# Kernel optimization log

Measured on AMD Instinct MI355X. Metric: run time of the kernel, lower is better.

Reference implementation:

```python
import jax, jax.numpy as jnp
import numpy as np

B, T, V, E, H = 4096, 128, 30, 256, 128

def setup_inputs() -> dict:
    key = jax.random.key(0)
    ks = jax.random.split(key, 12)
    inpt = jax.random.randint(ks[0], (B, T), 0, V, dtype=jnp.int32)
    h0 = jax.random.normal(ks[1], (B, H), dtype=jnp.float32)
    c0 = jax.random.normal(ks[2], (B, H), dtype=jnp.float32)
    mask_Y = jnp.ones((B, T), dtype=jnp.float32)
    s_e = 1.0
    s_l = 1.0 / np.sqrt(H)
    s_i = 1.0 / np.sqrt(E)
    emb = jax.random.normal(ks[3], (V, E), dtype=jnp.float32) * s_e
    W_ih = jax.random.normal(ks[4], (4 * H, E), dtype=jnp.float32) * s_i
    b_ih = jax.random.normal(ks[5], (4 * H,), dtype=jnp.float32) * s_i
    W_hh = jax.random.normal(ks[6], (4 * H, H), dtype=jnp.float32) * s_l
    b_hh = jax.random.normal(ks[7], (4 * H,), dtype=jnp.float32) * s_l
    W_lin = jax.random.normal(ks[8], (V, H), dtype=jnp.float32) * s_l
    b_lin = jax.random.normal(ks[9], (V,), dtype=jnp.float32) * s_l
    return {"inpt": inpt, "h0": h0, "c0": c0, "mask_Y": mask_Y, "beta": 1,
            "emb": emb, "W_ih": W_ih, "b_ih": b_ih, "W_hh": W_hh,
            "b_hh": b_hh, "W_lin": W_lin, "b_lin": b_lin}


def reference(inpt, h0, c0, mask_Y, beta, emb, W_ih, b_ih, W_hh, b_hh, W_lin, b_lin):
    # beta == 1 -> teacher forcing every step (u <= beta always), as in source.
    t_max = inpt.shape[1]
    # input tokens fed at steps t=0..t_max-2 are inpt[:, 0:t_max-1]
    x_emb = emb[inpt[:, :t_max - 1]]          # [B, T-1, E]
    xs = (jnp.swapaxes(x_emb, 0, 1),           # [T-1, B, E]
          inpt[:, 1:].T,                       # [T-1, B] true labels
          mask_Y[:, :t_max - 1].T)             # [T-1, B]

    def step(carry, xs_t):
        h, c = carry
        x, y, m = xs_t
        gates = x @ W_ih.T + b_ih + h @ W_hh.T + b_hh   # [B, 4H]
        i, f, g, o = jnp.split(gates, 4, axis=1)
        c2 = jax.nn.sigmoid(f) * c + jax.nn.sigmoid(i) * jnp.tanh(g)
        h2 = jax.nn.sigmoid(o) * jnp.tanh(c2)
        # -log(softmax(logits))[y] == -log_softmax(logits)[y]
        logp = jax.nn.log_softmax(h2 @ W_lin.T + b_lin, axis=1)  # [B, V]
        ce = -jnp.take_along_axis(logp, y[:, None], axis=1)[:, 0]
        return (h2, c2), jnp.sum(ce * m)

    _, step_losses = jax.lax.scan(step, (h0, c0), xs)
    return jnp.sum(step_losses) / jnp.sum(mask_Y)
```

## Files before the change

kernel.cpp:

```cpp
#include <hip/hip_runtime.h>


typedef __bf16 bf16x8 __attribute__((ext_vector_type(8)));
typedef float  f32x4  __attribute__((ext_vector_type(4)));

namespace {
constexpr int Bn = 4096, Tn = 128, Vn = 30, En = 256, Hn = 128, Gn = 512;
constexpr int WS_LOSS  = 0;
constexpr int WS_MASK  = 1;
constexpr int WS_XPROJ = 16;
constexpr int WS_WF_F  = WS_XPROJ + Vn * Gn;
}

__device__ __forceinline__ float fexp2(float x) { return __builtin_amdgcn_exp2f(x); }
__device__ __forceinline__ float frcp(float x)  { return __builtin_amdgcn_rcpf(x); }
__device__ __forceinline__ float sigf(float x)  { return frcp(1.f + fexp2(x * -1.44269504f)); }
__device__ __forceinline__ float tanh_(float x) { return 1.f - 2.f * frcp(fexp2(x * 2.88539008f) + 1.f); }

__global__ void k_wfrag(const float* __restrict__ W_hh, float* __restrict__ ws) {
  int fid = blockIdx.x * 256 + threadIdx.x;
  int l = fid & 63, kt = (fid >> 6) & 3, g = (fid >> 8) & 3, w = fid >> 10;
  int n  = (g * 8 + w) * 16 + (l & 15);
  int k0 = kt * 32 + (l >> 4) * 8;
  const float* src = W_hh + n * Hn + k0;
  union { __bf16 h[8]; uint4 u; } pk;
#pragma unroll
  for (int j = 0; j < 8; ++j) pk.h[j] = (__bf16)src[j];
  __bf16* wf = (__bf16*)(ws + WS_WF_F);
  *(uint4*)(wf + fid * 8) = pk.u;
}

__global__ void k_wlfrag(const float* __restrict__ W_lin, float* __restrict__ ws) {
  int fid = blockIdx.x * 256 + threadIdx.x;
  if (fid < 2) ws[fid] = 0.f;
  int l = fid & 63, kt = (fid >> 6) & 3, n = fid >> 8;
  int col = n * 16 + (l & 15);
  int k0  = kt * 32 + (l >> 4) * 8;
  union { __bf16 h[8]; uint4 u; } pk;
#pragma unroll
  for (int j = 0; j < 8; ++j)
    pk.h[j] = (col < Vn) ? (__bf16)W_lin[col * Hn + k0 + j] : (__bf16)0.f;
  __bf16* wf = (__bf16*)(ws + WS_WF_F);
  *(uint4*)(wf + 65536 + fid * 8) = pk.u;
}

__global__ void k_xproj(const float* __restrict__ emb, const float* __restrict__ W_ih,
                        const float* __restrict__ b_ih, const float* __restrict__ b_hh,
                        float* __restrict__ ws) {
  __shared__ __align__(16) float es[En];
  int v = blockIdx.x >> 1;
  int j = ((blockIdx.x & 1) << 8) + threadIdx.x;
  es[threadIdx.x] = emb[v * En + threadIdx.x];
  __syncthreads();
  float a = b_ih[j] + b_hh[j];
  const float* wr = W_ih + j * En;
#pragma unroll 4
  for (int e = 0; e < En; e += 4) {
    float4 w = *(const float4*)(wr + e);
    float4 x = *(const float4*)(es + e);
    a += x.x * w.x + x.y * w.y + x.z * w.z + x.w * w.w;
  }
  ws[WS_XPROJ + v * Gn + j] = a;
}

__global__ void k_mask(const float* __restrict__ m, float* __restrict__ ws) {
  float s = 0.f;
  for (int i = blockIdx.x * 256 + threadIdx.x; i < Bn * Tn; i += 128 * 256) s += m[i];
#pragma unroll
  for (int off = 32; off > 0; off >>= 1) s += __shfl_down(s, off, 64);
  __shared__ float r[4];
  int lane = threadIdx.x & 63, w = threadIdx.x >> 6;
  if (lane == 0) r[w] = s;
  __syncthreads();
  if (threadIdx.x == 0) atomicAdd(ws + WS_MASK, r[0] + r[1] + r[2] + r[3]);
}

__global__ __launch_bounds__(512, 1) void k_main(
    const int* __restrict__ inpt, const float* __restrict__ h0,
    const float* __restrict__ c0, const float* __restrict__ maskY,
    const float* __restrict__ b_lin, float* __restrict__ ws) {
  __shared__ __align__(16) __bf16 hbuf[2][16][136];
  __shared__ float logits[16][33];
  __shared__ int   tok[16][Tn];
  __shared__ float red[16];

  const float*  Xp  = ws + WS_XPROJ;
  const __bf16* wf  = (const __bf16*)(ws + WS_WF_F);
  const __bf16* wlf = wf + 65536;

  const int tid = threadIdx.x;
  const int w = tid >> 6, l = tid & 63, quad = l >> 4, lc = l & 15;
  const int row0 = blockIdx.x * 16;
  const int kh = w * 16 + lc;

  bf16x8 wfr[4][4];
#pragma unroll
  for (int g = 0; g < 4; ++g)
#pragma unroll
    for (int kt = 0; kt < 4; ++kt)
      wfr[g][kt] = __builtin_bit_cast(
          bf16x8, *(const uint4*)(wf + (((w * 4 + g) * 4 + kt) * 64 + l) * 8));

  bf16x8 wlr[4];
  if (w < 2) {
#pragma unroll
    for (int kt = 0; kt < 4; ++kt)
      wlr[kt] = __builtin_bit_cast(
          bf16x8, *(const uint4*)(wlf + ((w * 4 + kt) * 64 + l) * 8));
  }
  const float blv = (w < 2 && kh < Vn) ? b_lin[kh] : 0.f;

  for (int idx = tid; idx < 16 * Tn; idx += 512) {
    int r = idx >> 7, t = idx & 127;
    tok[r][t] = inpt[(row0 + r) * Tn + t];
  }
  for (int idx = tid; idx < 16 * Hn; idx += 512) {
    int r = idx >> 7, k = idx & 127;
    hbuf[0][r][k] = (__bf16)h0[(row0 + r) * Hn + k];
  }
  float creg[4];
#pragma unroll
  for (int p = 0; p < 4; ++p)
    creg[p] = c0[(row0 + quad * 4 + p) * Hn + kh];
  float ce_acc = 0.f;
  __syncthreads();

  int par = 0;
  for (int t = 0; t < Tn - 1; ++t) {
    const __bf16* hc = &hbuf[par][0][0];
    __bf16*       hn = &hbuf[par ^ 1][0][0];

    bf16x8 af[4];
#pragma unroll
    for (int kt = 0; kt < 4; ++kt)
      af[kt] = __builtin_bit_cast(
          bf16x8, *(const uint4*)(hc + lc * 136 + kt * 32 + quad * 8));

    float xv[4][4];
#pragma unroll
    for (int p = 0; p < 4; ++p) {
      const float* xr = Xp + tok[quad * 4 + p][t] * Gn + kh;
#pragma unroll
      for (int g = 0; g < 4; ++g) xv[p][g] = xr[g * 128];
    }

    f32x4 acc[4] = {{0, 0, 0, 0}, {0, 0, 0, 0}, {0, 0, 0, 0}, {0, 0, 0, 0}};
#pragma unroll
    for (int g = 0; g < 4; ++g)
#pragma unroll
      for (int kt = 0; kt < 4; ++kt)
        acc[g] = __builtin_amdgcn_mfma_f32_16x16x32_bf16(af[kt], wfr[g][kt], acc[g], 0, 0, 0);

#pragma unroll
    for (int p = 0; p < 4; ++p) {
      float gi = acc[0][p] + xv[p][0];
      float gf = acc[1][p] + xv[p][1];
      float gg = acc[2][p] + xv[p][2];
      float go = acc[3][p] + xv[p][3];
      float c2 = sigf(gf) * creg[p] + sigf(gi) * tanh_(gg);
      float h2 = sigf(go) * tanh_(c2);
      creg[p] = c2;
      hn[(quad * 4 + p) * 136 + kh] = (__bf16)h2;
    }
    __syncthreads();

    if (w < 2) {
      f32x4 lacc = {blv, blv, blv, blv};
#pragma unroll
      for (int kt = 0; kt < 4; ++kt) {
        bf16x8 a2 = __builtin_bit_cast(
            bf16x8, *(const uint4*)(hn + lc * 136 + kt * 32 + quad * 8));
        lacc = __builtin_amdgcn_mfma_f32_16x16x32_bf16(a2, wlr[kt], lacc, 0, 0, 0);
      }
      if (kh < Vn) {
#pragma unroll
        for (int p = 0; p < 4; ++p) logits[quad * 4 + p][kh] = lacc[p];
      }
    }
    __syncthreads();

    if (tid < 16) {
      float mx = -3.4e38f;
#pragma unroll
      for (int v = 0; v < Vn; ++v) mx = fmaxf(mx, logits[tid][v]);
      float s = 0.f;
#pragma unroll
      for (int v = 0; v < Vn; ++v) s += fexp2((logits[tid][v] - mx) * 1.44269504f);
      int y = tok[tid][t + 1];
      float ce = (mx + __logf(s)) - logits[tid][y];
      ce_acc += ce * maskY[(row0 + tid) * Tn + t];
    }
    par ^= 1;
  }

  if (tid < 16) red[tid] = ce_acc;
  __syncthreads();
  if (tid == 0) {
    float s = 0.f;
#pragma unroll
    for (int i = 0; i < 16; ++i) s += red[i];
    atomicAdd(ws + WS_LOSS, s);
  }
}

__global__ void k_final(const float* __restrict__ ws, float* __restrict__ out) {
  if (threadIdx.x == 0 && blockIdx.x == 0) out[0] = ws[WS_LOSS] / ws[WS_MASK];
}

extern "C" void kernel_launch(void* const* d_in, const int* in_sizes, int n_in,
                              void* d_out, int out_size, void* d_ws, size_t ws_size,
                              hipStream_t stream) {
  const int*   inpt  = (const int*)  d_in[0];
  const float* h0    = (const float*)d_in[1];
  const float* c0    = (const float*)d_in[2];
  const float* maskY = (const float*)d_in[3];
  const float* emb   = (const float*)d_in[5];
  const float* W_ih  = (const float*)d_in[6];
  const float* b_ih  = (const float*)d_in[7];
  const float* W_hh  = (const float*)d_in[8];
  const float* b_hh  = (const float*)d_in[9];
  const float* W_lin = (const float*)d_in[10];
  const float* b_lin = (const float*)d_in[11];
  float* ws  = (float*)d_ws;
  float* out = (float*)d_out;

  hipLaunchKernelGGL(k_wlfrag, dim3(2),   dim3(256), 0, stream, W_lin, ws);
  hipLaunchKernelGGL(k_wfrag,  dim3(32),  dim3(256), 0, stream, W_hh, ws);
  hipLaunchKernelGGL(k_xproj,  dim3(60),  dim3(256), 0, stream, emb, W_ih, b_ih, b_hh, ws);
  hipLaunchKernelGGL(k_mask,   dim3(128), dim3(256), 0, stream, maskY, ws);
  hipLaunchKernelGGL(k_main,   dim3(256), dim3(512), 0, stream, inpt, h0, c0, maskY, b_lin, ws);
  hipLaunchKernelGGL(k_final,  dim3(1),   dim3(64),  0, stream, ws, out);
}
```

Measured before the change: 272.0 us.

## Add dedicated softmax warp, fuse setup kernels, prefetch gate inputs, drop a barrier

```diff
diff --git a/kernel.cpp b/kernel.cpp
--- a/kernel.cpp
+++ b/kernel.cpp
@@ -17,74 +17,61 @@
 __device__ __forceinline__ float sigf(float x)  { return frcp(1.f + fexp2(x * -1.44269504f)); }
 __device__ __forceinline__ float tanh_(float x) { return 1.f - 2.f * frcp(fexp2(x * 2.88539008f) + 1.f); }
 
-__global__ void k_wfrag(const float* __restrict__ W_hh, float* __restrict__ ws) {
-  int fid = blockIdx.x * 256 + threadIdx.x;
-  int l = fid & 63, kt = (fid >> 6) & 3, g = (fid >> 8) & 3, w = fid >> 10;
-  int n  = (g * 8 + w) * 16 + (l & 15);
-  int k0 = kt * 32 + (l >> 4) * 8;
-  const float* src = W_hh + n * Hn + k0;
-  union { __bf16 h[8]; uint4 u; } pk;
-#pragma unroll
-  for (int j = 0; j < 8; ++j) pk.h[j] = (__bf16)src[j];
-  __bf16* wf = (__bf16*)(ws + WS_WF_F);
-  *(uint4*)(wf + fid * 8) = pk.u;
-}
-
-__global__ void k_wlfrag(const float* __restrict__ W_lin, float* __restrict__ ws) {
-  int fid = blockIdx.x * 256 + threadIdx.x;
-  if (fid < 2) ws[fid] = 0.f;
-  int l = fid & 63, kt = (fid >> 6) & 3, n = fid >> 8;
-  int col = n * 16 + (l & 15);
-  int k0  = kt * 32 + (l >> 4) * 8;
-  union { __bf16 h[8]; uint4 u; } pk;
-#pragma unroll
-  for (int j = 0; j < 8; ++j)
-    pk.h[j] = (col < Vn) ? (__bf16)W_lin[col * Hn + k0 + j] : (__bf16)0.f;
-  __bf16* wf = (__bf16*)(ws + WS_WF_F);
-  *(uint4*)(wf + 65536 + fid * 8) = pk.u;
-}
-
-__global__ void k_xproj(const float* __restrict__ emb, const float* __restrict__ W_ih,
+__global__ void k_setup(const float* __restrict__ emb, const float* __restrict__ W_ih,
                         const float* __restrict__ b_ih, const float* __restrict__ b_hh,
+                        const float* __restrict__ W_hh, const float* __restrict__ W_lin,
                         float* __restrict__ ws) {
-  __shared__ __align__(16) float es[En];
-  int v = blockIdx.x >> 1;
-  int j = ((blockIdx.x & 1) << 8) + threadIdx.x;
-  es[threadIdx.x] = emb[v * En + threadIdx.x];
-  __syncthreads();
-  float a = b_ih[j] + b_hh[j];
-  const float* wr = W_ih + j * En;
+  const int bid = blockIdx.x, tid = threadIdx.x;
+  if (bid < 60) {
+    __shared__ __align__(16) float es[En];
+    int v = bid >> 1;
+    int j = ((bid & 1) << 8) + tid;
+    es[tid] = emb[v * En + tid];
+    __syncthreads();
+    float a = b_ih[j] + b_hh[j];
+    const float* wr = W_ih + j * En;
 #pragma unroll 4
-  for (int e = 0; e < En; e += 4) {
-    float4 w = *(const float4*)(wr + e);
-    float4 x = *(const float4*)(es + e);
-    a += x.x * w.x + x.y * w.y + x.z * w.z + x.w * w.w;
-  }
-  ws[WS_XPROJ + v * Gn + j] = a;
-}
-
-__global__ void k_mask(const float* __restrict__ m, float* __restrict__ ws) {
-  float s = 0.f;
-  for (int i = blockIdx.x * 256 + threadIdx.x; i < Bn * Tn; i += 128 * 256) s += m[i];
-#pragma unroll
-  for (int off = 32; off > 0; off >>= 1) s += __shfl_down(s, off, 64);
-  __shared__ float r[4];
-  int lane = threadIdx.x & 63, w = threadIdx.x >> 6;
-  if (lane == 0) r[w] = s;
-  __syncthreads();
-  if (threadIdx.x == 0) atomicAdd(ws + WS_MASK, r[0] + r[1] + r[2] + r[3]);
-}
-
-__global__ __launch_bounds__(512, 1) void k_main(
+    for (int e = 0; e < En; e += 4) {
+      float4 w = *(const float4*)(wr + e);
+      float4 x = *(const float4*)(es + e);
+      a += x.x * w.x + x.y * w.y + x.z * w.z + x.w * w.w;
+    }
+    ws[WS_XPROJ + v * Gn + (j & 127) * 4 + (j >> 7)] = a;
+  } else if (bid < 92) {
+    int fid = (bid - 60) * 256 + tid;
+    int l = fid & 63, kt = (fid >> 6) & 3, g = (fid >> 8) & 3, w = fid >> 10;
+    int n  = (g * 8 + w) * 16 + (l & 15);
+    int k0 = kt * 32 + (l >> 4) * 8;
+    const float* src = W_hh + n * Hn + k0;
+    union { __bf16 h[8]; uint4 u; } pk;
+#pragma unroll
+    for (int j = 0; j < 8; ++j) pk.h[j] = (__bf16)src[j];
+    __bf16* wf = (__bf16*)(ws + WS_WF_F);
+    *(uint4*)(wf + fid * 8) = pk.u;
+  } else {
+    int fid = (bid - 92) * 256 + tid;
+    if (fid < 2) ws[fid] = 0.f;
+    int l = fid & 63, kt = (fid >> 6) & 3, n = fid >> 8;
+    int col = n * 16 + (l & 15);
+    int k0  = kt * 32 + (l >> 4) * 8;
+    union { __bf16 h[8]; uint4 u; } pk;
+#pragma unroll
+    for (int j = 0; j < 8; ++j)
+      pk.h[j] = (col < Vn) ? (__bf16)W_lin[col * Hn + k0 + j] : (__bf16)0.f;
+    __bf16* wf = (__bf16*)(ws + WS_WF_F);
+    *(uint4*)(wf + 65536 + fid * 8) = pk.u;
+  }
+}
+
+__global__ __launch_bounds__(576, 1) void k_main(
     const int* __restrict__ inpt, const float* __restrict__ h0,
     const float* __restrict__ c0, const float* __restrict__ maskY,
     const float* __restrict__ b_lin, float* __restrict__ ws) {
   __shared__ __align__(16) __bf16 hbuf[2][16][136];
-  __shared__ float logits[16][33];
-  __shared__ int   tok[16][Tn];
-  __shared__ float red[16];
+  __shared__ int tok[16][Tn];
 
   const float*  Xp  = ws + WS_XPROJ;
+  const float4* X4  = (const float4*)Xp;
   const __bf16* wf  = (const __bf16*)(ws + WS_WF_F);
   const __bf16* wlf = wf + 65536;
 
@@ -93,113 +80,138 @@
   const int row0 = blockIdx.x * 16;
   const int kh = w * 16 + lc;
 
-  bf16x8 wfr[4][4];
-#pragma unroll
-  for (int g = 0; g < 4; ++g)
-#pragma unroll
-    for (int kt = 0; kt < 4; ++kt)
-      wfr[g][kt] = __builtin_bit_cast(
-          bf16x8, *(const uint4*)(wf + (((w * 4 + g) * 4 + kt) * 64 + l) * 8));
-
-  bf16x8 wlr[4];
-  if (w < 2) {
-#pragma unroll
-    for (int kt = 0; kt < 4; ++kt)
-      wlr[kt] = __builtin_bit_cast(
-          bf16x8, *(const uint4*)(wlf + ((w * 4 + kt) * 64 + l) * 8));
-  }
-  const float blv = (w < 2 && kh < Vn) ? b_lin[kh] : 0.f;
-
-  for (int idx = tid; idx < 16 * Tn; idx += 512) {
+  for (int idx = tid; idx < 16 * Tn; idx += 576) {
     int r = idx >> 7, t = idx & 127;
     tok[r][t] = inpt[(row0 + r) * Tn + t];
   }
-  for (int idx = tid; idx < 16 * Hn; idx += 512) {
+  for (int idx = tid; idx < 16 * Hn; idx += 576) {
     int r = idx >> 7, k = idx & 127;
     hbuf[0][r][k] = (__bf16)h0[(row0 + r) * Hn + k];
   }
-  float creg[4];
-#pragma unroll
-  for (int p = 0; p < 4; ++p)
-    creg[p] = c0[(row0 + quad * 4 + p) * Hn + kh];
+
+  bf16x8 wfr[4][4];
+  float  creg[4];
+  bf16x8 wlr[4][2];
+  float  bias0 = 0.f, bias1 = 0.f, mloc = 0.f;
+  if (w < 8) {
+#pragma unroll
+    for (int g = 0; g < 4; ++g)
+#pragma unroll
+      for (int kt = 0; kt < 4; ++kt)
+        wfr[g][kt] = __builtin_bit_cast(
+            bf16x8, *(const uint4*)(wf + (((w * 4 + g) * 4 + kt) * 64 + l) * 8));
+#pragma unroll
+    for (int p = 0; p < 4; ++p)
+      creg[p] = c0[(row0 + quad * 4 + p) * Hn + kh];
+    if (w == 7) {
+      float s = 0.f;
+      const float4* m4 = (const float4*)(maskY + row0 * Tn);
+#pragma unroll
+      for (int i = 0; i < 8; ++i) s += m4[l + i * 64].x + m4[l + i * 64].y +
+                                       m4[l + i * 64].z + m4[l + i * 64].w;
+      mloc = s;
+    }
+  } else {
+#pragma unroll
+    for (int kt = 0; kt < 4; ++kt)
+#pragma unroll
+      for (int n = 0; n < 2; ++n)
+        wlr[kt][n] = __builtin_bit_cast(
+            bf16x8, *(const uint4*)(wlf + ((n * 4 + kt) * 64 + l) * 8));
+    bias0 = b_lin[lc];
+    bias1 = (lc + 16 < Vn) ? b_lin[lc + 16] : -1e30f;
+  }
   float ce_acc = 0.f;
   __syncthreads();
 
-  int par = 0;
+  float4 xv[4];
+  if (w < 8) {
+#pragma unroll
+    for (int p = 0; p < 4; ++p)
+      xv[p] = X4[tok[quad * 4 + p][0] * 128 + kh];
+  }
+
   for (int t = 0; t < Tn - 1; ++t) {
-    const __bf16* hc = &hbuf[par][0][0];
-    __bf16*       hn = &hbuf[par ^ 1][0][0];
-
-    bf16x8 af[4];
-#pragma unroll
-    for (int kt = 0; kt < 4; ++kt)
-      af[kt] = __builtin_bit_cast(
-          bf16x8, *(const uint4*)(hc + lc * 136 + kt * 32 + quad * 8));
-
-    float xv[4][4];
-#pragma unroll
-    for (int p = 0; p < 4; ++p) {
-      const float* xr = Xp + tok[quad * 4 + p][t] * Gn + kh;
-#pragma unroll
-      for (int g = 0; g < 4; ++g) xv[p][g] = xr[g * 128];
-    }
-
-    f32x4 acc[4] = {{0, 0, 0, 0}, {0, 0, 0, 0}, {0, 0, 0, 0}, {0, 0, 0, 0}};
-#pragma unroll
-    for (int g = 0; g < 4; ++g)
+    const int par = t & 1;
+    if (w < 8) {
+      const __bf16* hc = &hbuf[par][0][0];
+      __bf16*       hn = &hbuf[par ^ 1][0][0];
+
+      bf16x8 af[4];
 #pragma unroll
       for (int kt = 0; kt < 4; ++kt)
-        acc[g] = __builtin_amdgcn_mfma_f32_16x16x32_bf16(af[kt], wfr[g][kt], acc[g], 0, 0, 0);
-
-#pragma unroll
-    for (int p = 0; p < 4; ++p) {
-      float gi = acc[0][p] + xv[p][0];
-      float gf = acc[1][p] + xv[p][1];
-      float gg = acc[2][p] + xv[p][2];
-      float go = acc[3][p] + xv[p][3];
-      float c2 = sigf(gf) * creg[p] + sigf(gi) * tanh_(gg);
-      float h2 = sigf(go) * tanh_(c2);
-      creg[p] = c2;
-      hn[(quad * 4 + p) * 136 + kh] = (__bf16)h2;
+        af[kt] = __builtin_bit_cast(
+            bf16x8, *(const uint4*)(hc + lc * 136 + kt * 32 + quad * 8));
+
+      float4 xn[4];
+#pragma unroll
+      for (int p = 0; p < 4; ++p)
+        xn[p] = X4[tok[quad * 4 + p][t + 1] * 128 + kh];
+
+      f32x4 acc[4] = {{0, 0, 0, 0}, {0, 0, 0, 0}, {0, 0, 0, 0}, {0, 0, 0, 0}};
+#pragma unroll
+      for (int g = 0; g < 4; ++g)
+#pragma unroll
+        for (int kt = 0; kt < 4; ++kt)
+          acc[g] = __builtin_amdgcn_mfma_f32_16x16x32_bf16(af[kt], wfr[g][kt], acc[g], 0, 0, 0);
+
+#pragma unroll
+      for (int p = 0; p < 4; ++p) {
+        float gi = acc[0][p] + xv[p].x;
+        float gf = acc[1][p] + xv[p].y;
+        float gg = acc[2][p] + xv[p].z;
+        float go = acc[3][p] + xv[p].w;
+        float c2 = sigf(gf) * creg[p] + sigf(gi) * tanh_(gg);
+        float h2 = sigf(go) * tanh_(c2);
+        creg[p] = c2;
+        hn[(quad * 4 + p) * 136 + kh] = (__bf16)h2;
+        xv[p] = xn[p];
+      }
     }
     __syncthreads();
 
-    if (w < 2) {
-      f32x4 lacc = {blv, blv, blv, blv};
+    if (w == 8) {
+      const __bf16* hn = &hbuf[par ^ 1][0][0];
+      f32x4 lacc[2] = {{bias0, bias0, bias0, bias0}, {bias1, bias1, bias1, bias1}};
 #pragma unroll
       for (int kt = 0; kt < 4; ++kt) {
         bf16x8 a2 = __builtin_bit_cast(
             bf16x8, *(const uint4*)(hn + lc * 136 + kt * 32 + quad * 8));
-        lacc = __builtin_amdgcn_mfma_f32_16x16x32_bf16(a2, wlr[kt], lacc, 0, 0, 0);
+        lacc[0] = __builtin_amdgcn_mfma_f32_16x16x32_bf16(a2, wlr[kt][0], lacc[0], 0, 0, 0);
+        lacc[1] = __builtin_amdgcn_mfma_f32_16x16x32_bf16(a2, wlr[kt][1], lacc[1], 0, 0, 0);
       }
-      if (kh < Vn) {
-#pragma unroll
-        for (int p = 0; p < 4; ++p) logits[quad * 4 + p][kh] = lacc[p];
+#pragma unroll
+      for (int p = 0; p < 4; ++p) {
+        float a0 = lacc[0][p], a1 = lacc[1][p];
+        float m = fmaxf(a0, a1);
+        m = fmaxf(m, __shfl_xor(m, 1));
+        m = fmaxf(m, __shfl_xor(m, 2));
+        m = fmaxf(m, __shfl_xor(m, 4));
+        m = fmaxf(m, __shfl_xor(m, 8));
+        float e = fexp2((a0 - m) * 1.44269504f) + fexp2((a1 - m) * 1.44269504f);
+        e += __shfl_xor(e, 1);
+        e += __shfl_xor(e, 2);
+        e += __shfl_xor(e, 4);
+        e += __shfl_xor(e, 8);
+        int r = quad * 4 + p;
+        int y = tok[r][t + 1];
+        float sel = (y < 16) ? a0 : a1;
+        float ly = __shfl(sel, (l & 48) + (y & 15));
+        float ce = (m + __logf(e)) - ly;
+        if (lc == p) ce_acc += ce * maskY[(row0 + r) * Tn + t];
       }
     }
-    __syncthreads();
-
-    if (tid < 16) {
-      float mx = -3.4e38f;
-#pragma unroll
-      for (int v = 0; v < Vn; ++v) mx = fmaxf(mx, logits[tid][v]);
-      float s = 0.f;
-#pragma unroll
-      for (int v = 0; v < Vn; ++v) s += fexp2((logits[tid][v] - mx) * 1.44269504f);
-      int y = tok[tid][t + 1];
-      float ce = (mx + __logf(s)) - logits[tid][y];
-      ce_acc += ce * maskY[(row0 + tid) * Tn + t];
-    }
-    par ^= 1;
-  }
-
-  if (tid < 16) red[tid] = ce_acc;
-  __syncthreads();
-  if (tid == 0) {
-    float s = 0.f;
-#pragma unroll
-    for (int i = 0; i < 16; ++i) s += red[i];
-    atomicAdd(ws + WS_LOSS, s);
+  }
+
+  if (w == 8) {
+#pragma unroll
+    for (int off = 32; off > 0; off >>= 1) ce_acc += __shfl_down(ce_acc, off);
+    if (l == 0) atomicAdd(ws + WS_LOSS, ce_acc);
+  }
+  if (w == 7) {
+#pragma unroll
+    for (int off = 32; off > 0; off >>= 1) mloc += __shfl_down(mloc, off);
+    if (l == 0) atomicAdd(ws + WS_MASK, mloc);
   }
 }
 
@@ -224,10 +236,9 @@
   float* ws  = (float*)d_ws;
   float* out = (float*)d_out;
 
-  hipLaunchKernelGGL(k_wlfrag, dim3(2),   dim3(256), 0, stream, W_lin, ws);
-  hipLaunchKernelGGL(k_wfrag,  dim3(32),  dim3(256), 0, stream, W_hh, ws);
-  hipLaunchKernelGGL(k_xproj,  dim3(60),  dim3(256), 0, stream, emb, W_ih, b_ih, b_hh, ws);
-  hipLaunchKernelGGL(k_mask,   dim3(128), dim3(256), 0, stream, maskY, ws);
-  hipLaunchKernelGGL(k_main,   dim3(256), dim3(512), 0, stream, inpt, h0, c0, maskY, b_lin, ws);
-  hipLaunchKernelGGL(k_final,  dim3(1),   dim3(64),  0, stream, ws, out);
-}
+  hipLaunchKernelGGL(k_setup, dim3(94),  dim3(256), 0, stream,
+                     emb, W_ih, b_ih, b_hh, W_hh, W_lin, ws);
+  hipLaunchKernelGGL(k_main,  dim3(256), dim3(576), 0, stream,
+                     inpt, h0, c0, maskY, b_lin, ws);
+  hipLaunchKernelGGL(k_final, dim3(1),   dim3(64),  0, stream, ws, out);
+}
```

Measured after the change: 381.6 us. 40.3% more time.
